# Kernel optimization log

Measured on AMD Instinct MI355X. Metric: run time of the kernel, lower is better.

## Reference

```python
import math
import jax, jax.numpy as jnp
import numpy as np

B_SZ, N_TOK, D_MODEL, EXPAND, D_STATE = 4, 1024, 192, 2, 16
D_INNER = EXPAND * D_MODEL  # 384


def setup_inputs() -> dict:
    key = jax.random.key(0)
    ks = jax.random.split(key, 6)
    dt_init = math.log(math.exp(0.1) - 1.0)
    x = jax.random.normal(ks[0], (B_SZ, N_TOK, D_INNER), dtype=jnp.float32)
    # dt projection weights: uniform(-1e-4, 1e-4), bias = softplus-inverse(0.1)
    W_dts = jax.random.uniform(ks[1], (D_INNER, D_INNER), minval=-1e-4, maxval=1e-4, dtype=jnp.float32)
    W_dtd = jax.random.uniform(ks[2], (D_INNER, D_INNER), minval=-1e-4, maxval=1e-4, dtype=jnp.float32)
    b_dts = jnp.full((D_INNER,), dt_init, dtype=jnp.float32)
    b_dtd = jnp.full((D_INNER,), dt_init, dtype=jnp.float32)
    # B/C projections (no bias)
    W_B = jax.random.normal(ks[3], (D_STATE, D_INNER), dtype=jnp.float32) * 0.05
    W_C = jax.random.normal(ks[4], (D_STATE, D_INNER), dtype=jnp.float32) * 0.05
    D_param = jnp.ones((D_INNER,), dtype=jnp.float32)
    A_log = jnp.broadcast_to(jnp.log(jnp.arange(1, D_STATE + 1, dtype=jnp.float32))[None, :], (D_INNER, D_STATE))
    diff_raw = jnp.zeros((1, D_INNER, 1, 1), dtype=jnp.float32)
    return {"x": x, "W_dts": W_dts, "b_dts": b_dts, "W_dtd": W_dtd, "b_dtd": b_dtd,
            "W_B": W_B, "W_C": W_C, "D_param": D_param, "A_log": A_log,
            "diff_raw": diff_raw, "K_steps": 3}


def _laplacian(h, H, W):
    # h: (B, N, D, S); 5-point stencil with replicate (edge) padding, per (D,S) channel
    Bv, N, D, S = h.shape
    g = h.reshape(Bv, H, W, D, S)
    g = jnp.pad(g, ((0, 0), (1, 1), (1, 1), (0, 0), (0, 0)), mode='edge')
    lap = (g[:, 2:, 1:-1] + g[:, :-2, 1:-1] + g[:, 1:-1, 2:] + g[:, 1:-1, :-2]
           - 4.0 * g[:, 1:-1, 1:-1])
    return lap.reshape(Bv, N, D, S)


def reference(x, W_dts, b_dts, W_dtd, b_dtd, W_B, W_C, D_param, A_log, diff_raw, K_steps):
    Bv, N, D = x.shape
    H = Wd = int(math.sqrt(N))
    A = -jax.nn.softplus(A_log)                                   # (D, S), negative decay
    delta_s = jnp.minimum(jax.nn.softplus(x @ W_dts.T + b_dts), 0.15)  # (B, N, D)
    delta_d = jnp.minimum(jax.nn.softplus(x @ W_dtd.T + b_dtd), 0.15)  # (B, N, D)
    B_mat = x @ W_B.T                                             # (B, N, S)
    C_mat = x @ W_C.T                                             # (B, N, S)
    h0 = jnp.einsum('bnd,bns->bnds', x, B_mat)                    # (B, N, D, S)
    D_coeff = (jax.nn.sigmoid(diff_raw) * 0.5).reshape(1, 1, D, 1)
    dt = 1.0 / K_steps
    A_exp = A[None, None]            # (1, 1, D, S)
    ds_e = delta_s[..., None]        # (B, N, D, 1)
    dd_e = delta_d[..., None]
    h = h0
    for _ in range(K_steps):
        lap = _laplacian(h, H, Wd)
        h = h + dt * (ds_e * (A_exp * h + h0) + dd_e * D_coeff * lap)
    y = jnp.einsum('bnds,bns->bnd', h, C_mat) + x * D_param
    return y
```

## Files before the change

kernel.cpp:

```cpp
#include <hip/hip_runtime.h>
#include <hip/hip_bf16.h>

#define BSZ   4
#define NTOK  1024
#define DIN   384
#define DST   16
#define MROWS (BSZ * NTOK)
#define KDIM  384
#define NM    (MROWS * DIN)

typedef __attribute__((ext_vector_type(8))) short bf16x8;
typedef __attribute__((ext_vector_type(4))) float f32x4;

__device__ __forceinline__ float softplus_f(float z) {
  return (z > 20.0f) ? z : log1pf(expf(z));
}

__device__ __forceinline__ unsigned short f32_to_bf16(float f) {
  unsigned int u = __float_as_uint(f);
  unsigned int rnd = 0x7fffu + ((u >> 16) & 1u);
  return (unsigned short)((u + rnd) >> 16);
}

__device__ __forceinline__ float bf16_lo(unsigned int w) { return __uint_as_float(w << 16); }
__device__ __forceinline__ float bf16_hi(unsigned int w) { return __uint_as_float(w & 0xffff0000u); }

__global__ __launch_bounds__(256) void prep_kernel(
    const float* __restrict__ x, float* __restrict__ xT,
    unsigned short* __restrict__ xb,
    const float* __restrict__ Wdts, const float* __restrict__ Wdtd,
    const float* __restrict__ WB,   const float* __restrict__ WC,
    unsigned short* __restrict__ Wb)
{
  if (blockIdx.z == 4) {
    const int lin = blockIdx.y * 32 + blockIdx.x;
    if (lin >= 156) return;
    const int idx8 = (lin * 256 + threadIdx.x) * 8;
    const int row = idx8 / KDIM;
    const int k   = idx8 % KDIM;
    uint4 o = make_uint4(0u, 0u, 0u, 0u);
    if (row < 800) {
      const float* src;
      if (row < 384)      src = Wdts + (long)row * KDIM + k;
      else if (row < 768) src = Wdtd + (long)(row - 384) * KDIM + k;
      else if (row < 784) src = WB   + (long)(row - 768) * KDIM + k;
      else                src = WC   + (long)(row - 784) * KDIM + k;
      float4 v0 = *(const float4*)src;
      float4 v1 = *(const float4*)(src + 4);
      o.x = (unsigned int)f32_to_bf16(v0.x) | ((unsigned int)f32_to_bf16(v0.y) << 16);
      o.y = (unsigned int)f32_to_bf16(v0.z) | ((unsigned int)f32_to_bf16(v0.w) << 16);
      o.z = (unsigned int)f32_to_bf16(v1.x) | ((unsigned int)f32_to_bf16(v1.y) << 16);
      o.w = (unsigned int)f32_to_bf16(v1.z) | ((unsigned int)f32_to_bf16(v1.w) << 16);
    }
    *(uint4*)&Wb[idx8] = o;
    return;
  }
  __shared__ float tile[32][33];
  const int n0 = blockIdx.x * 32;
  const int d0 = blockIdx.y * 32;
  const int b  = blockIdx.z;
  const int tx = threadIdx.x & 31, ty = threadIdx.x >> 5;
#pragma unroll
  for (int i = 0; i < 4; ++i) {
    int nn = n0 + ty + i * 8;
    float v = x[(long)(b * NTOK + nn) * DIN + d0 + tx];
    tile[ty + i * 8][tx] = v;
    xb[(long)(b * NTOK + nn) * DIN + d0 + tx] = f32_to_bf16(v);
  }
  __syncthreads();
#pragma unroll
  for (int i = 0; i < 4; ++i) {
    int dd = d0 + ty + i * 8;
    xT[(long)(b * DIN + dd) * NTOK + n0 + tx] = tile[tx][ty + i * 8];
  }
}

#define AREAD(MAT, ROW, KO) \
  (*(const bf16x8*)&(MAT)[(ROW) * 64 + ((((KO) >> 3) ^ ((ROW) & 7)) << 3)])

__global__ __launch_bounds__(256) void proj_mfma_kernel(
    const unsigned short* __restrict__ xb,
    const unsigned short* __restrict__ Wb,
    const float* __restrict__ bdts, const float* __restrict__ bdtd,
    unsigned short* __restrict__ dsT, unsigned short* __restrict__ ddT,
    float* __restrict__ BT, float* __restrict__ CT)
{
  __shared__ short smem_s[2][2][64 * 64];

  const int t    = threadIdx.x;
  const int bm   = blockIdx.x & 63;
  const int bn   = blockIdx.x >> 6;
  const int row0 = bm * 64;
  const int col0 = bn * 64;
  const int bat  = row0 >> 10;
  const int n0   = row0 & 1023;

  const int l  = t & 63;
  const int w  = t >> 6;
  const int wr = (w >> 1) * 32;
  const int wc = (w & 1) * 32;
  const int lr = l & 15;
  const int lk = (l >> 4) * 8;

  const int s0 = t,       r0 = s0 >> 3;
  const int s1 = 256 + t, r1 = s1 >> 3;
  const int j0 = ((s0 & 7) ^ (r0 & 7)) << 3;
  const int j1 = ((s1 & 7) ^ (r1 & 7)) << 3;
  const int wb0 = (t & 192) * 8;
  const int wb1 = (256 + (t & 192)) * 8;

#define STAGEM(LBASE, GSRC)                                                \
  {                                                                        \
    __builtin_amdgcn_global_load_lds(                                      \
        (const void*)((GSRC) + (long)r0 * KDIM + j0),                      \
        (void*)((LBASE) + wb0), 16, 0, 0);                                 \
    __builtin_amdgcn_global_load_lds(                                      \
        (const void*)((GSRC) + (long)r1 * KDIM + j1),                      \
        (void*)((LBASE) + wb1), 16, 0, 0);                                 \
  }

  f32x4 acc[2][2];
  const f32x4 zero = {0.f, 0.f, 0.f, 0.f};
  acc[0][0] = zero; acc[0][1] = zero; acc[1][0] = zero; acc[1][1] = zero;

  const unsigned short* Ag = xb + (long)row0 * KDIM;
  const unsigned short* Wg = Wb + (long)col0 * KDIM;

  STAGEM(smem_s[0][0], Ag);
  STAGEM(smem_s[0][1], Wg);

  for (int it = 0; it < 6; ++it) {
    const int cur = it & 1;
    __syncthreads();
    if (it + 1 < 6) {
      const int k0n = (it + 1) * 64;
      STAGEM(smem_s[cur ^ 1][0], Ag + k0n);
      STAGEM(smem_s[cur ^ 1][1], Wg + k0n);
    }
    const short* Asm = smem_s[cur][0];
    const short* Wsm = smem_s[cur][1];
#pragma unroll
    for (int kh = 0; kh < 2; ++kh) {
      const int ko = kh * 32 + lk;
      bf16x8 a0 = AREAD(Asm, wr + lr, ko);
      bf16x8 a1 = AREAD(Asm, wr + 16 + lr, ko);
      bf16x8 b0 = AREAD(Wsm, wc + lr, ko);
      bf16x8 b1 = AREAD(Wsm, wc + 16 + lr, ko);
      acc[0][0] = __builtin_amdgcn_mfma_f32_16x16x32_bf16(a0, b0, acc[0][0], 0, 0, 0);
      acc[0][1] = __builtin_amdgcn_mfma_f32_16x16x32_bf16(a0, b1, acc[0][1], 0, 0, 0);
      acc[1][0] = __builtin_amdgcn_mfma_f32_16x16x32_bf16(a1, b0, acc[1][0], 0, 0, 0);
      acc[1][1] = __builtin_amdgcn_mfma_f32_16x16x32_bf16(a1, b1, acc[1][1], 0, 0, 0);
    }
  }
#undef STAGEM

  if (bn < 12) {
    const float* bias = (bn < 6) ? bdts : bdtd;
    unsigned short* plane = (bn < 6) ? dsT : ddT;
    const int dbase = (bn < 6) ? col0 : col0 - 384;
    const float bv0 = bias[dbase + wc + lr];
    const float bv1 = bias[dbase + wc + 16 + lr];
    __syncthreads();
    unsigned short* outl = (unsigned short*)smem_s;
#pragma unroll
    for (int i = 0; i < 2; ++i)
#pragma unroll
      for (int j = 0; j < 2; ++j) {
        const float bb = j ? bv1 : bv0;
        const int cl = wc + j * 16 + lr;
#pragma unroll
        for (int q = 0; q < 4; ++q) {
          const int nl = wr + i * 16 + (l >> 4) * 4 + q;
          float dl = fminf(softplus_f(acc[i][j][q] + bb), 0.15f);
          outl[cl * 72 + nl] = f32_to_bf16(dl);
        }
      }
    __syncthreads();
    const int dl = t >> 2;
    const int seg = t & 3;
    uint4 w0 = *(const uint4*)&outl[dl * 72 + seg * 16];
    uint4 w1 = *(const uint4*)&outl[dl * 72 + seg * 16 + 8];
    long addr = (long)(bat * DIN + dbase + dl) * NTOK + n0 + seg * 16;
    *(uint4*)&plane[addr]     = w0;
    *(uint4*)&plane[addr + 8] = w1;
  } else {
#pragma unroll
    for (int i = 0; i < 2; ++i)
#pragma unroll
      for (int j = 0; j < 2; ++j) {
        const int cl = wc + j * 16 + lr;
        const int rowbase = row0 + wr + i * 16 + (l >> 4) * 4;
        if (cl < 16)       *(f32x4*)&BT[(long)cl * MROWS + rowbase] = acc[i][j];
        else if (cl < 32)  *(f32x4*)&CT[(long)(cl - 16) * MROWS + rowbase] = acc[i][j];
      }
  }
}

__global__ __launch_bounds__(256) void ssm_kernel(
    const float* __restrict__ xT,
    const unsigned short* __restrict__ dsT,
    const unsigned short* __restrict__ ddT,
    const float* __restrict__ BT, const float* __restrict__ CT,
    const float* __restrict__ Alog,
    const float* __restrict__ diffraw, const int* __restrict__ Kp,
    unsigned short* __restrict__ yQ0, unsigned short* __restrict__ yQ1,
    unsigned short* __restrict__ yQ2, unsigned short* __restrict__ yQ3)
{
  __shared__ float P[4 * 1024];
  const int bid  = blockIdx.x;
  const int sq   = bid / (BSZ * DIN);
  const int bd   = bid % (BSZ * DIN);
  const int d = bd % DIN;
  const int b = bd / DIN;
  const int t   = threadIdx.x;
  const int s   = sq * 4 + (t >> 6);
  const int l64 = t & 63;
  const int pr  = l64 >> 3, pc = l64 & 7;
  const int K = Kp[0];
  const float dt = 1.0f / (float)K;
  const float Dc = 0.5f / (1.0f + expf(-diffraw[d]));
  const float A  = -log1pf(expf(Alog[d * DST + s]));
  const float dtDc = dt * Dc;
  const long col = (long)(b * DIN + d) * NTOK;
  const long gr0 = (long)b * NTOK;
  const int  c0  = pc * 4;

  float4 cv[4];
#pragma unroll
  for (int i = 0; i < 4; ++i)
    cv[i] = *(const float4*)&CT[(long)s * MROWS + gr0 + (pr * 4 + i) * 32 + c0];

  float h[16], cA[16], g0[16], a2v[16];
#pragma unroll
  for (int i = 0; i < 4; ++i) {
    const int n = (pr * 4 + i) * 32 + c0;
    float4 xv = *(const float4*)&xT[col + n];
    float4 bv = *(const float4*)&BT[(long)s * MROWS + gr0 + n];
    uint2 dsw = *(const uint2*)&dsT[col + n];
    uint2 ddw = *(const uint2*)&ddT[col + n];
    float dsf[4] = { bf16_lo(dsw.x), bf16_hi(dsw.x), bf16_lo(dsw.y), bf16_hi(dsw.y) };
    float ddf[4] = { bf16_lo(ddw.x), bf16_hi(ddw.x), bf16_lo(ddw.y), bf16_hi(ddw.y) };
    float xa[4] = { xv.x, xv.y, xv.z, xv.w };
    float ba[4] = { bv.x, bv.y, bv.z, bv.w };
#pragma unroll
    for (int j = 0; j < 4; ++j) {
      const int e = i * 4 + j;
      float a1 = dt * dsf[j];
      float a2 = dtDc * ddf[j];
      float h0 = xa[j] * ba[j];
      h[e]   = h0;
      g0[e]  = a1 * h0;
      a2v[e] = a2;
      cA[e]  = fmaf(a1, A, 1.0f) - 4.0f * a2;
    }
  }

  const int lu = (l64 - 8) & 63, ld = (l64 + 8) & 63;
  const int ll = (l64 - 1) & 63, lrr = (l64 + 1) & 63;

  for (int k = 0; k < K; ++k) {
    float up[4], dn[4], lf[4], rt[4];
#pragma unroll
    for (int j = 0; j < 4; ++j) {
      up[j] = __shfl(h[12 + j], lu);
      dn[j] = __shfl(h[j], ld);
      lf[j] = __shfl(h[4 * j + 3], ll);
      rt[j] = __shfl(h[4 * j], lrr);
    }
#pragma unroll
    for (int j = 0; j < 4; ++j) {
      up[j] = (pr == 0) ? h[j]          : up[j];
      dn[j] = (pr == 7) ? h[12 + j]     : dn[j];
      lf[j] = (pc == 0) ? h[4 * j]      : lf[j];
      rt[j] = (pc == 7) ? h[4 * j + 3]  : rt[j];
    }
    float hn[16];
#pragma unroll
    for (int i = 0; i < 4; ++i)
#pragma unroll
      for (int j = 0; j < 4; ++j) {
        const int e = i * 4 + j;
        float uv = (i == 0) ? up[j] : h[e - 4];
        float dv = (i == 3) ? dn[j] : h[e + 4];
        float lv = (j == 0) ? lf[i] : h[e - 1];
        float rv = (j == 3) ? rt[i] : h[e + 1];
        float S  = (uv + dv) + (lv + rv);
        hn[e] = fmaf(cA[e], h[e], fmaf(a2v[e], S, g0[e]));
      }
#pragma unroll
    for (int e = 0; e < 16; ++e) h[e] = hn[e];
  }

  const int sw = t >> 6;
#pragma unroll
  for (int i = 0; i < 4; ++i) {
    const int n = (pr * 4 + i) * 32 + c0;
    float4 pv;
    pv.x = h[i * 4 + 0] * cv[i].x;
    pv.y = h[i * 4 + 1] * cv[i].y;
    pv.z = h[i * 4 + 2] * cv[i].z;
    pv.w = h[i * 4 + 3] * cv[i].w;
    *(float4*)&P[sw * 1024 + n] = pv;
  }
  __syncthreads();

  unsigned short* yQ = (sq == 0) ? yQ0 : (sq == 1) ? yQ1 : (sq == 2) ? yQ2 : yQ3;
#pragma unroll
  for (int j = 0; j < 4; ++j) {
    const int n = t + j * 256;
    float sum = P[n] + P[1024 + n] + P[2048 + n] + P[3072 + n];
    yQ[col + n] = f32_to_bf16(sum);
  }
}

__global__ __launch_bounds__(256) void untranspose_kernel(
    const unsigned short* __restrict__ yQ0, const unsigned short* __restrict__ yQ1,
    const unsigned short* __restrict__ yQ2, const unsigned short* __restrict__ yQ3,
    const float* __restrict__ xT, const float* __restrict__ Dparam,
    float* __restrict__ out)
{
  __shared__ float tile[32][33];
  const int n0 = blockIdx.x * 32;
  const int d0 = blockIdx.y * 32;
  const int b  = blockIdx.z;
  const int tx = threadIdx.x & 31, ty = threadIdx.x >> 5;
#pragma unroll
  for (int i = 0; i < 4; ++i) {
    int dd = d0 + ty + i * 8;
    long idx = (long)(b * DIN + dd) * NTOK + n0 + tx;
    float v0 = __uint_as_float((unsigned int)yQ0[idx] << 16);
    float v1 = __uint_as_float((unsigned int)yQ1[idx] << 16);
    float v2 = __uint_as_float((unsigned int)yQ2[idx] << 16);
    float v3 = __uint_as_float((unsigned int)yQ3[idx] << 16);
    tile[ty + i * 8][tx] = ((v0 + v1) + (v2 + v3)) + xT[idx] * Dparam[dd];
  }
  __syncthreads();
#pragma unroll
  for (int i = 0; i < 4; ++i) {
    int nn = n0 + ty + i * 8;
    out[(long)(b * NTOK + nn) * DIN + d0 + tx] = tile[tx][ty + i * 8];
  }
}

extern "C" void kernel_launch(void* const* d_in, const int* in_sizes, int n_in,
                              void* d_out, int out_size, void* d_ws, size_t ws_size,
                              hipStream_t stream) {
  const float* x     = (const float*)d_in[0];
  const float* Wdts  = (const float*)d_in[1];
  const float* bdts  = (const float*)d_in[2];
  const float* Wdtd  = (const float*)d_in[3];
  const float* bdtd  = (const float*)d_in[4];
  const float* WB    = (const float*)d_in[5];
  const float* WC    = (const float*)d_in[6];
  const float* Dpar  = (const float*)d_in[7];
  const float* Alog  = (const float*)d_in[8];
  const float* diffr = (const float*)d_in[9];
  const int*   Kst   = (const int*)d_in[10];

  float* BT = (float*)d_ws;
  float* CT = BT + (long)DST * MROWS;
  float* xT = CT + (long)DST * MROWS;
  unsigned short* yQ0 = (unsigned short*)(xT + NM);
  unsigned short* yQ1 = yQ0 + NM;
  unsigned short* yQ2 = yQ1 + NM;
  unsigned short* yQ3 = yQ2 + NM;
  unsigned short* xb  = yQ0;
  unsigned short* Wb  = xb + NM;

  unsigned short* dsT = (unsigned short*)d_out;
  unsigned short* ddT = dsT + NM;

  prep_kernel<<<dim3(NTOK / 32, DIN / 32, BSZ + 1), dim3(256), 0, stream>>>(
      x, xT, xb, Wdts, Wdtd, WB, WC, Wb);

  proj_mfma_kernel<<<dim3(64 * 13), dim3(256), 0, stream>>>(
      xb, Wb, bdts, bdtd, dsT, ddT, BT, CT);

  ssm_kernel<<<dim3(BSZ * DIN * 4), dim3(256), 0, stream>>>(
      xT, dsT, ddT, BT, CT, Alog, diffr, Kst, yQ0, yQ1, yQ2, yQ3);

  untranspose_kernel<<<dim3(NTOK / 32, DIN / 32, BSZ), dim3(256), 0, stream>>>(
      yQ0, yQ1, yQ2, yQ3, xT, Dpar, (float*)d_out);
}
```

Baseline: 62.67 us.

## Store transposed x and B/C projections as bf16, reorder SSM blocks

Transposed x and the B/C projection outputs are now stored as bf16 rather than fp32, halving their workspace traffic in the prep, projection and SSM kernels. The final untranspose kernel reads the original fp32 x directly in row-major layout for the D skip term, so the skip path keeps full precision. SSM block indices are remapped so the four state-quarter blocks of each (batch, channel) pair run next to each other, which may improve cache reuse of shared inputs. The cost is extra rounding error in h0 and the C contraction.

Result: no change. 63.57 us (+1.4%).

```diff
diff --git a/kernel.cpp b/kernel.cpp
--- a/kernel.cpp
+++ b/kernel.cpp
@@ -22,11 +22,15 @@
   return (unsigned short)((u + rnd) >> 16);
 }
 
+__device__ __forceinline__ unsigned int pack_bf16x2(float a, float b) {
+  return (unsigned int)f32_to_bf16(a) | ((unsigned int)f32_to_bf16(b) << 16);
+}
+
 __device__ __forceinline__ float bf16_lo(unsigned int w) { return __uint_as_float(w << 16); }
 __device__ __forceinline__ float bf16_hi(unsigned int w) { return __uint_as_float(w & 0xffff0000u); }
 
 __global__ __launch_bounds__(256) void prep_kernel(
-    const float* __restrict__ x, float* __restrict__ xT,
+    const float* __restrict__ x, unsigned short* __restrict__ xTb,
     unsigned short* __restrict__ xb,
     const float* __restrict__ Wdts, const float* __restrict__ Wdtd,
     const float* __restrict__ WB,   const float* __restrict__ WC,
@@ -47,10 +51,10 @@
       else                src = WC   + (long)(row - 784) * KDIM + k;
       float4 v0 = *(const float4*)src;
       float4 v1 = *(const float4*)(src + 4);
-      o.x = (unsigned int)f32_to_bf16(v0.x) | ((unsigned int)f32_to_bf16(v0.y) << 16);
-      o.y = (unsigned int)f32_to_bf16(v0.z) | ((unsigned int)f32_to_bf16(v0.w) << 16);
-      o.z = (unsigned int)f32_to_bf16(v1.x) | ((unsigned int)f32_to_bf16(v1.y) << 16);
-      o.w = (unsigned int)f32_to_bf16(v1.z) | ((unsigned int)f32_to_bf16(v1.w) << 16);
+      o.x = pack_bf16x2(v0.x, v0.y);
+      o.y = pack_bf16x2(v0.z, v0.w);
+      o.z = pack_bf16x2(v1.x, v1.y);
+      o.w = pack_bf16x2(v1.z, v1.w);
     }
     *(uint4*)&Wb[idx8] = o;
     return;
@@ -71,7 +75,7 @@
 #pragma unroll
   for (int i = 0; i < 4; ++i) {
     int dd = d0 + ty + i * 8;
-    xT[(long)(b * DIN + dd) * NTOK + n0 + tx] = tile[tx][ty + i * 8];
+    xTb[(long)(b * DIN + dd) * NTOK + n0 + tx] = f32_to_bf16(tile[tx][ty + i * 8]);
   }
 }
 
@@ -83,7 +87,7 @@
     const unsigned short* __restrict__ Wb,
     const float* __restrict__ bdts, const float* __restrict__ bdtd,
     unsigned short* __restrict__ dsT, unsigned short* __restrict__ ddT,
-    float* __restrict__ BT, float* __restrict__ CT)
+    unsigned short* __restrict__ BTb, unsigned short* __restrict__ CTb)
 {
   __shared__ short smem_s[2][2][64 * 64];
 
@@ -190,26 +194,31 @@
       for (int j = 0; j < 2; ++j) {
         const int cl = wc + j * 16 + lr;
         const int rowbase = row0 + wr + i * 16 + (l >> 4) * 4;
-        if (cl < 16)       *(f32x4*)&BT[(long)cl * MROWS + rowbase] = acc[i][j];
-        else if (cl < 32)  *(f32x4*)&CT[(long)(cl - 16) * MROWS + rowbase] = acc[i][j];
+        uint2 o;
+        o.x = pack_bf16x2(acc[i][j][0], acc[i][j][1]);
+        o.y = pack_bf16x2(acc[i][j][2], acc[i][j][3]);
+        if (cl < 16)       *(uint2*)&BTb[(long)cl * MROWS + rowbase] = o;
+        else if (cl < 32)  *(uint2*)&CTb[(long)(cl - 16) * MROWS + rowbase] = o;
       }
   }
 }
 
 __global__ __launch_bounds__(256) void ssm_kernel(
-    const float* __restrict__ xT,
+    const unsigned short* __restrict__ xTb,
     const unsigned short* __restrict__ dsT,
     const unsigned short* __restrict__ ddT,
-    const float* __restrict__ BT, const float* __restrict__ CT,
+    const unsigned short* __restrict__ BTb, const unsigned short* __restrict__ CTb,
     const float* __restrict__ Alog,
     const float* __restrict__ diffraw, const int* __restrict__ Kp,
     unsigned short* __restrict__ yQ0, unsigned short* __restrict__ yQ1,
     unsigned short* __restrict__ yQ2, unsigned short* __restrict__ yQ3)
 {
   __shared__ float P[4 * 1024];
-  const int bid  = blockIdx.x;
-  const int sq   = bid / (BSZ * DIN);
-  const int bd   = bid % (BSZ * DIN);
+  const int bid = blockIdx.x;
+  const int grp = bid >> 5;
+  const int wi  = bid & 31;
+  const int sq  = wi >> 3;
+  const int bd  = grp * 8 + (wi & 7);
   const int d = bd % DIN;
   const int b = bd / DIN;
   const int t   = threadIdx.x;
@@ -225,23 +234,23 @@
   const long gr0 = (long)b * NTOK;
   const int  c0  = pc * 4;
 
-  float4 cv[4];
+  uint2 cw[4];
 #pragma unroll
   for (int i = 0; i < 4; ++i)
-    cv[i] = *(const float4*)&CT[(long)s * MROWS + gr0 + (pr * 4 + i) * 32 + c0];
+    cw[i] = *(const uint2*)&CTb[(long)s * MROWS + gr0 + (pr * 4 + i) * 32 + c0];
 
   float h[16], cA[16], g0[16], a2v[16];
 #pragma unroll
   for (int i = 0; i < 4; ++i) {
     const int n = (pr * 4 + i) * 32 + c0;
-    float4 xv = *(const float4*)&xT[col + n];
-    float4 bv = *(const float4*)&BT[(long)s * MROWS + gr0 + n];
+    uint2 xw  = *(const uint2*)&xTb[col + n];
+    uint2 bw  = *(const uint2*)&BTb[(long)s * MROWS + gr0 + n];
     uint2 dsw = *(const uint2*)&dsT[col + n];
     uint2 ddw = *(const uint2*)&ddT[col + n];
+    float xa[4]  = { bf16_lo(xw.x),  bf16_hi(xw.x),  bf16_lo(xw.y),  bf16_hi(xw.y) };
+    float ba[4]  = { bf16_lo(bw.x),  bf16_hi(bw.x),  bf16_lo(bw.y),  bf16_hi(bw.y) };
     float dsf[4] = { bf16_lo(dsw.x), bf16_hi(dsw.x), bf16_lo(dsw.y), bf16_hi(dsw.y) };
     float ddf[4] = { bf16_lo(ddw.x), bf16_hi(ddw.x), bf16_lo(ddw.y), bf16_hi(ddw.y) };
-    float xa[4] = { xv.x, xv.y, xv.z, xv.w };
-    float ba[4] = { bv.x, bv.y, bv.z, bv.w };
 #pragma unroll
     for (int j = 0; j < 4; ++j) {
       const int e = i * 4 + j;
@@ -296,10 +305,10 @@
   for (int i = 0; i < 4; ++i) {
     const int n = (pr * 4 + i) * 32 + c0;
     float4 pv;
-    pv.x = h[i * 4 + 0] * cv[i].x;
-    pv.y = h[i * 4 + 1] * cv[i].y;
-    pv.z = h[i * 4 + 2] * cv[i].z;
-    pv.w = h[i * 4 + 3] * cv[i].w;
+    pv.x = h[i * 4 + 0] * bf16_lo(cw[i].x);
+    pv.y = h[i * 4 + 1] * bf16_hi(cw[i].x);
+    pv.z = h[i * 4 + 2] * bf16_lo(cw[i].y);
+    pv.w = h[i * 4 + 3] * bf16_hi(cw[i].y);
     *(float4*)&P[sw * 1024 + n] = pv;
   }
   __syncthreads();
@@ -316,7 +325,7 @@
 __global__ __launch_bounds__(256) void untranspose_kernel(
     const unsigned short* __restrict__ yQ0, const unsigned short* __restrict__ yQ1,
     const unsigned short* __restrict__ yQ2, const unsigned short* __restrict__ yQ3,
-    const float* __restrict__ xT, const float* __restrict__ Dparam,
+    const float* __restrict__ x, const float* __restrict__ Dparam,
     float* __restrict__ out)
 {
   __shared__ float tile[32][33];
@@ -332,13 +341,15 @@
     float v1 = __uint_as_float((unsigned int)yQ1[idx] << 16);
     float v2 = __uint_as_float((unsigned int)yQ2[idx] << 16);
     float v3 = __uint_as_float((unsigned int)yQ3[idx] << 16);
-    tile[ty + i * 8][tx] = ((v0 + v1) + (v2 + v3)) + xT[idx] * Dparam[dd];
+    tile[ty + i * 8][tx] = (v0 + v1) + (v2 + v3);
   }
   __syncthreads();
+  const float Dp = Dparam[d0 + tx];
 #pragma unroll
   for (int i = 0; i < 4; ++i) {
     int nn = n0 + ty + i * 8;
-    out[(long)(b * NTOK + nn) * DIN + d0 + tx] = tile[tx][ty + i * 8];
+    long ix = (long)(b * NTOK + nn) * DIN + d0 + tx;
+    out[ix] = fmaf(x[ix], Dp, tile[tx][ty + i * 8]);
   }
 }
 
@@ -357,10 +368,10 @@
   const float* diffr = (const float*)d_in[9];
   const int*   Kst   = (const int*)d_in[10];
 
-  float* BT = (float*)d_ws;
-  float* CT = BT + (long)DST * MROWS;
-  float* xT = CT + (long)DST * MROWS;
-  unsigned short* yQ0 = (unsigned short*)(xT + NM);
+  unsigned short* BTb = (unsigned short*)d_ws;
+  unsigned short* CTb = BTb + (long)DST * MROWS;
+  unsigned short* xTb = CTb + (long)DST * MROWS;
+  unsigned short* yQ0 = xTb + NM;
   unsigned short* yQ1 = yQ0 + NM;
   unsigned short* yQ2 = yQ1 + NM;
   unsigned short* yQ3 = yQ2 + NM;
@@ -371,14 +382,14 @@
   unsigned short* ddT = dsT + NM;
 
   prep_kernel<<<dim3(NTOK / 32, DIN / 32, BSZ + 1), dim3(256), 0, stream>>>(
-      x, xT, xb, Wdts, Wdtd, WB, WC, Wb);
+      x, xTb, xb, Wdts, Wdtd, WB, WC, Wb);
 
   proj_mfma_kernel<<<dim3(64 * 13), dim3(256), 0, stream>>>(
-      xb, Wb, bdts, bdtd, dsT, ddT, BT, CT);
+      xb, Wb, bdts, bdtd, dsT, ddT, BTb, CTb);
 
   ssm_kernel<<<dim3(BSZ * DIN * 4), dim3(256), 0, stream>>>(
-      xT, dsT, ddT, BT, CT, Alog, diffr, Kst, yQ0, yQ1, yQ2, yQ3);
+      xTb, dsT, ddT, BTb, CTb, Alog, diffr, Kst, yQ0, yQ1, yQ2, yQ3);
 
   untranspose_kernel<<<dim3(NTOK / 32, DIN / 32, BSZ), dim3(256), 0, stream>>>(
-      yQ0, yQ1, yQ2, yQ3, xT, Dpar, (float*)d_out);
-}
+      yQ0, yQ1, yQ2, yQ3, x, Dpar, (float*)d_out);
+}
```
